# Optimization experiments

Hardware: AMD Instinct MI355X
Metric: run time of the kernel (lower is better)

Reference implementation:

```python
import jax, jax.numpy as jnp
import numpy as np

SUBSTEPS = 2  # fixed Tsit5 substeps per observation interval (replaces diffrax adaptive PID control)
# Tsit5 Butcher tableau (same stage math as diffrax.Tsit5)
C2, C3, C4, C5, C6 = 0.161, 0.327, 0.9, 0.9800255409045097, 1.0
A21 = 0.161
A31, A32 = -0.008480655492356989, 0.335480655492357
A41, A42, A43 = 2.8971530571054935, -6.359448489975075, 4.3622954328695815
A51, A52, A53, A54 = 5.325864828439257, -11.748883564062828, 7.4955393428898365, -0.09249506636175525
A61, A62, A63, A64, A65 = 5.86145544294642, -12.92096931784711, 8.159367898576159, -0.071584973281401, -0.028269050394068383
B1, B2, B3, B4, B5, B6 = 0.09646076681806523, 0.01, 0.4798896504144996, 1.379008574103742, -3.290069515436081, 2.324710524099774


def setup_inputs() -> dict:
    key = jax.random.key(0)
    ks = jax.random.split(key, 12)
    B, N, D_IN, H, ST, SW, OW, D_OUT = 128, 64, 32, 128, 16, 256, 256, 16

    def lin(k, o, i):
        return jax.random.normal(k, (o, i), jnp.float32) / np.sqrt(i).astype(np.float32)

    # strictly increasing timestamps with small intervals
    dts = jax.random.uniform(ks[0], (B, N), jnp.float32) * 0.05 + 0.01
    ts_batch = jnp.cumsum(dts, axis=1)
    X_batch = jax.random.normal(ks[1], (B, N, D_IN), jnp.float32)
    Static_batch = jax.random.normal(ks[2], (B, ST), jnp.float32)
    return dict(
        ts_batch=ts_batch, X_batch=X_batch, Static_batch=Static_batch,
        ode_w0=lin(ks[3], SW, 1 + H), ode_b0=jnp.zeros(SW, jnp.float32),
        ode_w1=lin(ks[4], SW, SW), ode_b1=jnp.zeros(SW, jnp.float32),
        ode_w2=lin(ks[5], H, SW), ode_b2=jnp.zeros(H, jnp.float32),
        ode_scale=jnp.array(1.0, jnp.float32),
        rnn_wh=lin(ks[6], H, H), rnn_wx=lin(ks[7], H, D_IN), rnn_bx=jnp.zeros(H, jnp.float32),
        inj_w=lin(ks[8], H, H + ST), inj_b=jnp.zeros(H, jnp.float32),
        out_w0=lin(ks[9], OW, H), out_b0=jnp.zeros(OW, jnp.float32),
        out_w1=lin(ks[10], OW, OW), out_b1=jnp.zeros(OW, jnp.float32),
        out_w2=lin(ks[11], D_OUT, OW), out_b2=jnp.zeros(D_OUT, jnp.float32),
    )


def reference(ts_batch, X_batch, Static_batch,
              ode_w0, ode_b0, ode_w1, ode_b1, ode_w2, ode_b2, ode_scale,
              rnn_wh, rnn_wx, rnn_bx, inj_w, inj_b,
              out_w0, out_b0, out_w1, out_b1, out_w2, out_b2):
    def f(t, h):  # vector field: t (B,), h (B,H)
        z = jnp.concatenate([t[:, None], h], axis=-1)
        z = jax.nn.silu(z @ ode_w0.T + ode_b0)
        z = jax.nn.silu(z @ ode_w1.T + ode_b1)
        return ode_scale * jnp.tanh(z @ ode_w2.T + ode_b2)

    def tsit5_step(t, dt, y):  # one Tsit5 step, batched over B
        d = dt[:, None]
        k1 = f(t, y)
        k2 = f(t + C2 * dt, y + d * (A21 * k1))
        k3 = f(t + C3 * dt, y + d * (A31 * k1 + A32 * k2))
        k4 = f(t + C4 * dt, y + d * (A41 * k1 + A42 * k2 + A43 * k3))
        k5 = f(t + C5 * dt, y + d * (A51 * k1 + A52 * k2 + A53 * k3 + A54 * k4))
        k6 = f(t + C6 * dt, y + d * (A61 * k1 + A62 * k2 + A63 * k3 + A64 * k4 + A65 * k5))
        return y + d * (B1 * k1 + B2 * k2 + B3 * k3 + B4 * k4 + B5 * k5 + B6 * k6)

    def ode_solve(t0, t1, y):  # fixed-substep Tsit5 integration from t0 to t1 (per-batch times)
        dt = (t1 - t0) / SUBSTEPS
        def body(yc, i):
            t = t0 + i.astype(t0.dtype) * dt
            return tsit5_step(t, dt, yc), None
        y, _ = jax.lax.scan(body, y, jnp.arange(SUBSTEPS))
        return y

    def rnn(h_prime, x):
        return jnp.tanh(h_prime @ rnn_wh.T + x @ rnn_wx.T + rnn_bx)

    # h0: rnn_cell(zeros, x0) -> inject static -> tanh
    h0 = jnp.tanh(X_batch[:, 0] @ rnn_wx.T + rnn_bx)  # hidden_linear(0) == 0
    h0 = jnp.tanh(jnp.concatenate([h0, Static_batch], axis=-1) @ inj_w.T + inj_b)

    xs = (ts_batch[:, :-1].T, ts_batch[:, 1:].T, jnp.swapaxes(X_batch[:, 1:], 0, 1))
    def step(h, inp):
        tp, tn, x = inp
        hp = ode_solve(tp, tn, h)
        return rnn(hp, x), None
    hN, _ = jax.lax.scan(step, h0, xs)

    z = jnp.tanh(hN @ out_w0.T + out_b0)
    z = jnp.tanh(z @ out_w1.T + out_b1)
    return z @ out_w2.T + out_b2  # (B, output_dim)
```

## Files before the change

### kernel.cpp

```cpp
#include <hip/hip_runtime.h>

typedef _Float16 f16;
typedef _Float16 f16x8 __attribute__((ext_vector_type(8)));
typedef float f32x4 __attribute__((ext_vector_type(4)));

#define MFMA16(a, b, c) __builtin_amdgcn_mfma_f32_16x16x32_f16((a), (b), (c), 0, 0, 0)

#define A21f 0.161f
#define A31f (-0.008480655492356989f)
#define A32f 0.335480655492357f
#define A41f 2.8971530571054935f
#define A42f (-6.359448489975075f)
#define A43f 4.3622954328695815f
#define A51f 5.325864828439257f
#define A52f (-11.748883564062828f)
#define A53f 7.4955393428898365f
#define A54f (-0.09249506636175525f)
#define A61f 5.86145544294642f
#define A62f (-12.92096931784711f)
#define A63f 8.159367898576159f
#define A64f (-0.071584973281401f)
#define A65f (-0.028269050394068383f)
#define B1f 0.09646076681806523f
#define B2f 0.01f
#define B3f 0.4798896504144996f
#define B4f 1.379008574103742f
#define B5f (-3.290069515436081f)
#define B6f 2.324710524099774f
#define C2f 0.161f
#define C3f 0.327f
#define C4f 0.9f
#define C5f 0.9800255409045097f
#define C6f 1.0f

#define PY 272
#define PZ 528
#define PX 80
#define PW 272
#define LDS_Y   0
#define LDS_Z1  4352
#define LDS_Z2  12800
#define LDS_X   21248
#define LDS_TS  22528
#define LDS_WH  26624
#define LDS_TOT 61440

__device__ __forceinline__ int yoff(int row, int bc)  { return LDS_Y  + row * PY + bc; }
__device__ __forceinline__ int z1off(int row, int bc) { return LDS_Z1 + row * PZ + bc; }
__device__ __forceinline__ int z2off(int row, int bc) { return LDS_Z2 + row * PZ + bc; }
__device__ __forceinline__ int xoff(int row, int bc)  { return LDS_X  + row * PX + bc; }
__device__ __forceinline__ int whoff(int row, int bc) { return LDS_WH + row * PW + bc; }

__device__ __forceinline__ float tanh_fast(float x) {
  return 2.0f * __builtin_amdgcn_rcpf(1.0f + __expf(-2.0f * x)) - 1.0f;
}
__device__ __forceinline__ float siluf(float x) {
  return x * __builtin_amdgcn_rcpf(1.0f + __expf(-x));
}

__global__ __launch_bounds__(512, 2)
void ode_rnn_kernel(const float* __restrict__ ts, const float* __restrict__ Xg,
                    const float* __restrict__ Sg,
                    const float* __restrict__ w0g, const float* __restrict__ b0g,
                    const float* __restrict__ w1g, const float* __restrict__ b1g,
                    const float* __restrict__ w2g, const float* __restrict__ b2g,
                    const float* __restrict__ scaleg,
                    const float* __restrict__ whg, const float* __restrict__ wxg,
                    const float* __restrict__ bxg,
                    const float* __restrict__ injwg, const float* __restrict__ injbg,
                    const float* __restrict__ ow0g, const float* __restrict__ ob0g,
                    const float* __restrict__ ow1g, const float* __restrict__ ob1g,
                    const float* __restrict__ ow2g, const float* __restrict__ ob2g,
                    float* __restrict__ outg) {
  const int t  = threadIdx.x;
  const int w  = t >> 6;
  const int l  = t & 63;
  const int lr = l & 15;
  const int lg = l >> 4;
  const int rb = blockIdx.x * 16;
  const int c1 = w * 32;
  const int c3 = w * 16;

  __shared__ __align__(16) unsigned char lds[LDS_TOT];

  for (int e = t; e < 16 * 64; e += 512) {
    *(float*)(lds + LDS_TS + e * 4) = ts[(size_t)(rb + (e >> 6)) * 64 + (e & 63)];
  }
  for (int e = t; e < 128 * 128; e += 512) {
    int r = e >> 7, c = e & 127;
    *(f16*)(lds + whoff(r, c * 2)) = (f16)whg[e];
  }
  {
    int r = t >> 5, d = t & 31;
    *(f16*)(lds + xoff(r, d * 2)) = (f16)Xg[(size_t)(rb + r) * 2048 + d];
  }
  if (t < 256) {
    int r = t >> 4, c = t & 15;
    *(f16*)(lds + z1off(r, (128 + c) * 2)) = (f16)Sg[(size_t)(rb + r) * 16 + c];
    *(f16*)(lds + z1off(r, (144 + c) * 2)) = (f16)0.0f;
  }

  float b0v[2], w0c0[2], b1v[2];
  #pragma unroll
  for (int nt = 0; nt < 2; ++nt) {
    int col = c1 + nt * 16 + lr;
    b0v[nt]  = b0g[col];
    w0c0[nt] = w0g[(size_t)col * 129];
    b1v[nt]  = b1g[col];
  }
  const float b2v = b2g[c3 + lr];
  const float bxv = bxg[c3 + lr];
  const float scalev = scaleg[0];

  auto ldfrag = [](const float* p) {
    f16x8 v;
    #pragma unroll
    for (int j = 0; j < 8; ++j) v[j] = (f16)p[j];
    return v;
  };

  f16x8 W0f[4][2];
  #pragma unroll
  for (int kt = 0; kt < 4; ++kt)
    #pragma unroll
    for (int nt = 0; nt < 2; ++nt)
      W0f[kt][nt] = ldfrag(w0g + (size_t)(c1 + nt * 16 + lr) * 129 + 1 + kt * 32 + lg * 8);

  f16x8 W1f[8][2];
  #pragma unroll
  for (int kt = 0; kt < 8; ++kt)
    #pragma unroll
    for (int nt = 0; nt < 2; ++nt)
      W1f[kt][nt] = ldfrag(w1g + (size_t)(c1 + nt * 16 + lr) * 256 + kt * 32 + lg * 8);

  f16x8 W2f[8];
  #pragma unroll
  for (int kt = 0; kt < 8; ++kt)
    W2f[kt] = ldfrag(w2g + (size_t)(c3 + lr) * 256 + kt * 32 + lg * 8);

  f16x8 WXf = ldfrag(wxg + (size_t)(c3 + lr) * 32 + lg * 8);

  __syncthreads();

  float y[4];
  float tpv[4], dv[4];

  auto writeY = [&](const float* yv) {
    #pragma unroll
    for (int r = 0; r < 4; ++r)
      *(f16*)(lds + yoff(lg * 4 + r, (c3 + lr) * 2)) = (f16)yv[r];
  };

  {
    f16x8 xa = *(const f16x8*)(lds + xoff(lr, lg * 16));
    f32x4 acc = {};
    acc = MFMA16(xa, WXf, acc);
    #pragma unroll
    for (int r = 0; r < 4; ++r) {
      float v = tanh_fast(acc[r] + bxv);
      *(f16*)(lds + z1off(lg * 4 + r, (c3 + lr) * 2)) = (f16)v;
    }
  }
  __syncthreads();
  {
    f16x8 af[5];
    #pragma unroll
    for (int kt = 0; kt < 5; ++kt) af[kt] = *(const f16x8*)(lds + z1off(lr, kt * 64 + lg * 16));
    f32x4 acc = {};
    int orow = c3 + lr;
    #pragma unroll
    for (int kt = 0; kt < 5; ++kt) {
      f16x8 bf;
      #pragma unroll
      for (int j = 0; j < 8; ++j) {
        int k = kt * 32 + lg * 8 + j;
        bf[j] = (k < 144) ? (f16)injwg[(size_t)orow * 144 + k] : (f16)0.0f;
      }
      acc = MFMA16(af[kt], bf, acc);
    }
    float ib = injbg[orow];
    #pragma unroll
    for (int r = 0; r < 4; ++r) y[r] = tanh_fast(acc[r] + ib);
  }
  writeY(y);
  __syncthreads();

  auto feval = [&](float sc, float* ko) {
    f16x8 af[8];
    #pragma unroll
    for (int kt = 0; kt < 4; ++kt) af[kt] = *(const f16x8*)(lds + yoff(lr, kt * 64 + lg * 16));
    f32x4 a1[2] = {}, a1b[2] = {};
    __builtin_amdgcn_s_setprio(1);
    #pragma unroll
    for (int kt = 0; kt < 2; ++kt)
      #pragma unroll
      for (int nt = 0; nt < 2; ++nt) {
        a1[nt]  = MFMA16(af[kt],     W0f[kt][nt],     a1[nt]);
        a1b[nt] = MFMA16(af[kt + 2], W0f[kt + 2][nt], a1b[nt]);
      }
    __builtin_amdgcn_s_setprio(0);
    #pragma unroll
    for (int nt = 0; nt < 2; ++nt)
      #pragma unroll
      for (int r = 0; r < 4; ++r) {
        float tr = tpv[r] + sc * dv[r];
        float v = siluf(a1[nt][r] + a1b[nt][r] + tr * w0c0[nt] + b0v[nt]);
        *(f16*)(lds + z1off(lg * 4 + r, (c1 + nt * 16 + lr) * 2)) = (f16)v;
      }
    __syncthreads();
    #pragma unroll
    for (int kt = 0; kt < 8; ++kt) af[kt] = *(const f16x8*)(lds + z1off(lr, kt * 64 + lg * 16));
    f32x4 a2[2] = {}, a2b[2] = {};
    __builtin_amdgcn_s_setprio(1);
    #pragma unroll
    for (int kt = 0; kt < 4; ++kt)
      #pragma unroll
      for (int nt = 0; nt < 2; ++nt) {
        a2[nt]  = MFMA16(af[kt],     W1f[kt][nt],     a2[nt]);
        a2b[nt] = MFMA16(af[kt + 4], W1f[kt + 4][nt], a2b[nt]);
      }
    __builtin_amdgcn_s_setprio(0);
    #pragma unroll
    for (int nt = 0; nt < 2; ++nt)
      #pragma unroll
      for (int r = 0; r < 4; ++r) {
        float v = siluf(a2[nt][r] + a2b[nt][r] + b1v[nt]);
        *(f16*)(lds + z2off(lg * 4 + r, (c1 + nt * 16 + lr) * 2)) = (f16)v;
      }
    __syncthreads();
    #pragma unroll
    for (int kt = 0; kt < 8; ++kt) af[kt] = *(const f16x8*)(lds + z2off(lr, kt * 64 + lg * 16));
    f32x4 a3 = {}, a3b = {}, a3c = {}, a3d = {};
    __builtin_amdgcn_s_setprio(1);
    #pragma unroll
    for (int kt = 0; kt < 2; ++kt) {
      a3  = MFMA16(af[kt],     W2f[kt],     a3);
      a3b = MFMA16(af[kt + 2], W2f[kt + 2], a3b);
      a3c = MFMA16(af[kt + 4], W2f[kt + 4], a3c);
      a3d = MFMA16(af[kt + 6], W2f[kt + 6], a3d);
    }
    __builtin_amdgcn_s_setprio(0);
    #pragma unroll
    for (int r = 0; r < 4; ++r)
      ko[r] = scalev * tanh_fast(((a3[r] + a3b[r]) + (a3c[r] + a3d[r])) + b2v);
  };

  #pragma unroll 1
  for (int n = 0; n < 63; ++n) {
    #pragma unroll
    for (int r = 0; r < 4; ++r) {
      float tp = *(const float*)(lds + LDS_TS + (((lg * 4 + r) * 64) + n) * 4);
      float tn = *(const float*)(lds + LDS_TS + (((lg * 4 + r) * 64) + n + 1) * 4);
      tpv[r] = tp;
      dv[r] = (tn - tp) * 0.5f;
    }
    {
      int r = t >> 5, d = t & 31;
      *(f16*)(lds + xoff(r, d * 2)) = (f16)Xg[(size_t)(rb + r) * 2048 + (size_t)(n + 1) * 32 + d];
    }

    #pragma unroll 1
    for (int s = 0; s < 2; ++s) {
      float k1v[4], k2v[4], k3v[4], k4v[4], k5v[4], k6v[4], yt[4];
      float sf = (float)s;
      feval(sf, k1v);
      #pragma unroll
      for (int i = 0; i < 4; ++i) yt[i] = y[i] + dv[i] * (A21f * k1v[i]);
      writeY(yt); __syncthreads();
      feval(sf + C2f, k2v);
      #pragma unroll
      for (int i = 0; i < 4; ++i) yt[i] = y[i] + dv[i] * (A31f * k1v[i] + A32f * k2v[i]);
      writeY(yt); __syncthreads();
      feval(sf + C3f, k3v);
      #pragma unroll
      for (int i = 0; i < 4; ++i) yt[i] = y[i] + dv[i] * (A41f * k1v[i] + A42f * k2v[i] + A43f * k3v[i]);
      writeY(yt); __syncthreads();
      feval(sf + C4f, k4v);
      #pragma unroll
      for (int i = 0; i < 4; ++i) yt[i] = y[i] + dv[i] * (A51f * k1v[i] + A52f * k2v[i] + A53f * k3v[i] + A54f * k4v[i]);
      writeY(yt); __syncthreads();
      feval(sf + C5f, k5v);
      #pragma unroll
      for (int i = 0; i < 4; ++i) yt[i] = y[i] + dv[i] * (A61f * k1v[i] + A62f * k2v[i] + A63f * k3v[i] + A64f * k4v[i] + A65f * k5v[i]);
      writeY(yt); __syncthreads();
      feval(sf + C6f, k6v);
      #pragma unroll
      for (int i = 0; i < 4; ++i)
        y[i] += dv[i] * (B1f * k1v[i] + B2f * k2v[i] + B3f * k3v[i] + B4f * k4v[i] + B5f * k5v[i] + B6f * k6v[i]);
      writeY(y); __syncthreads();
    }

    {
      f16x8 ha[4];
      #pragma unroll
      for (int kt = 0; kt < 4; ++kt) ha[kt] = *(const f16x8*)(lds + yoff(lr, kt * 64 + lg * 16));
      f16x8 xa = *(const f16x8*)(lds + xoff(lr, lg * 16));
      f32x4 acc = {}, accb = {};
      __builtin_amdgcn_s_setprio(1);
      #pragma unroll
      for (int kt = 0; kt < 2; ++kt) {
        f16x8 bf  = *(const f16x8*)(lds + whoff(c3 + lr, kt * 64 + lg * 16));
        f16x8 bf2 = *(const f16x8*)(lds + whoff(c3 + lr, (kt + 2) * 64 + lg * 16));
        acc  = MFMA16(ha[kt],     bf,  acc);
        accb = MFMA16(ha[kt + 2], bf2, accb);
      }
      acc = MFMA16(xa, WXf, acc);
      __builtin_amdgcn_s_setprio(0);
      #pragma unroll
      for (int r = 0; r < 4; ++r) y[r] = tanh_fast(acc[r] + accb[r] + bxv);
      writeY(y);
      __syncthreads();
    }
  }

  auto ldfrag2 = [](const float* p) {
    f16x8 v;
    #pragma unroll
    for (int j = 0; j < 8; ++j) v[j] = (f16)p[j];
    return v;
  };
  {
    f16x8 ha[4];
    #pragma unroll
    for (int kt = 0; kt < 4; ++kt) ha[kt] = *(const f16x8*)(lds + yoff(lr, kt * 64 + lg * 16));
    f32x4 acc[2] = {};
    #pragma unroll
    for (int kt = 0; kt < 4; ++kt)
      #pragma unroll
      for (int nt = 0; nt < 2; ++nt) {
        f16x8 bf = ldfrag2(ow0g + (size_t)(c1 + nt * 16 + lr) * 128 + kt * 32 + lg * 8);
        acc[nt] = MFMA16(ha[kt], bf, acc[nt]);
      }
    #pragma unroll
    for (int nt = 0; nt < 2; ++nt) {
      float bb = ob0g[c1 + nt * 16 + lr];
      #pragma unroll
      for (int r = 0; r < 4; ++r) {
        float v = tanh_fast(acc[nt][r] + bb);
        *(f16*)(lds + z1off(lg * 4 + r, (c1 + nt * 16 + lr) * 2)) = (f16)v;
      }
    }
  }
  __syncthreads();
  {
    f16x8 za[8];
    #pragma unroll
    for (int kt = 0; kt < 8; ++kt) za[kt] = *(const f16x8*)(lds + z1off(lr, kt * 64 + lg * 16));
    f32x4 acc[2] = {};
    #pragma unroll
    for (int kt = 0; kt < 8; ++kt)
      #pragma unroll
      for (int nt = 0; nt < 2; ++nt) {
        f16x8 bf = ldfrag2(ow1g + (size_t)(c1 + nt * 16 + lr) * 256 + kt * 32 + lg * 8);
        acc[nt] = MFMA16(za[kt], bf, acc[nt]);
      }
    #pragma unroll
    for (int nt = 0; nt < 2; ++nt) {
      float bb = ob1g[c1 + nt * 16 + lr];
      #pragma unroll
      for (int r = 0; r < 4; ++r) {
        float v = tanh_fast(acc[nt][r] + bb);
        *(f16*)(lds + z2off(lg * 4 + r, (c1 + nt * 16 + lr) * 2)) = (f16)v;
      }
    }
  }
  __syncthreads();
  if (w == 0) {
    f16x8 za[8];
    #pragma unroll
    for (int kt = 0; kt < 8; ++kt) za[kt] = *(const f16x8*)(lds + z2off(lr, kt * 64 + lg * 16));
    f32x4 acc = {};
    #pragma unroll
    for (int kt = 0; kt < 8; ++kt) {
      f16x8 bf = ldfrag2(ow2g + (size_t)lr * 256 + kt * 32 + lg * 8);
      acc = MFMA16(za[kt], bf, acc);
    }
    float bb = ob2g[lr];
    #pragma unroll
    for (int r = 0; r < 4; ++r)
      outg[(size_t)(rb + lg * 4 + r) * 16 + lr] = acc[r] + bb;
  }
}

extern "C" void kernel_launch(void* const* d_in, const int* in_sizes, int n_in,
                              void* d_out, int out_size, void* d_ws, size_t ws_size,
                              hipStream_t stream) {
  (void)in_sizes; (void)n_in; (void)d_ws; (void)ws_size; (void)out_size;
  ode_rnn_kernel<<<dim3(8), dim3(512), 0, stream>>>(
      (const float*)d_in[0],  (const float*)d_in[1],  (const float*)d_in[2],
      (const float*)d_in[3],  (const float*)d_in[4],  (const float*)d_in[5],
      (const float*)d_in[6],  (const float*)d_in[7],  (const float*)d_in[8],
      (const float*)d_in[9],  (const float*)d_in[10], (const float*)d_in[11],
      (const float*)d_in[12], (const float*)d_in[13], (const float*)d_in[14],
      (const float*)d_in[15], (const float*)d_in[16], (const float*)d_in[17],
      (const float*)d_in[18], (const float*)d_in[19], (const float*)d_in[20],
      (float*)d_out);
}
```

Before: 1.279 ms.

## Re-layout LDS activation and weight buffers into MFMA-fragment-contiguous blocks

Replaces the padded row-major LDS layouts for hidden state, intermediate activations, inputs and the recurrent weight with a blocked layout: 16 rows by 8 halves, stored so each lane's f16x8 fragment is one contiguous 16-byte chunk addressed by lane*16. Fragment reads become linear per wavefront and the scattered f16 writes are reorganised to match, aiming to cut LDS bank conflicts and address arithmetic in the latency-bound recurrent loop. The padding goes away, so LDS use shrinks a little. The scalar 2-byte stores remain and may still conflict.

```diff
diff --git a/kernel.cpp b/kernel.cpp
--- a/kernel.cpp
+++ b/kernel.cpp
@@ -33,23 +33,13 @@
 #define C5f 0.9800255409045097f
 #define C6f 1.0f
 
-#define PY 272
-#define PZ 528
-#define PX 80
-#define PW 272
 #define LDS_Y   0
-#define LDS_Z1  4352
-#define LDS_Z2  12800
-#define LDS_X   21248
-#define LDS_TS  22528
-#define LDS_WH  26624
-#define LDS_TOT 61440
-
-__device__ __forceinline__ int yoff(int row, int bc)  { return LDS_Y  + row * PY + bc; }
-__device__ __forceinline__ int z1off(int row, int bc) { return LDS_Z1 + row * PZ + bc; }
-__device__ __forceinline__ int z2off(int row, int bc) { return LDS_Z2 + row * PZ + bc; }
-__device__ __forceinline__ int xoff(int row, int bc)  { return LDS_X  + row * PX + bc; }
-__device__ __forceinline__ int whoff(int row, int bc) { return LDS_WH + row * PW + bc; }
+#define LDS_Z1  4096
+#define LDS_Z2  12288
+#define LDS_X   20480
+#define LDS_TS  21504
+#define LDS_WH  25600
+#define LDS_TOT 58368
 
 __device__ __forceinline__ float tanh_fast(float x) {
   return 2.0f * __builtin_amdgcn_rcpf(1.0f + __expf(-2.0f * x)) - 1.0f;
@@ -83,21 +73,28 @@
 
   __shared__ __align__(16) unsigned char lds[LDS_TOT];
 
+  const int ard  = l * 16;
+  const int whrd = LDS_WH + lg * 2048 + w * 256 + lr * 16;
+  const int zw   = w * 1024 + (lr >> 3) * 256 + lg * 64 + (lr & 7) * 2;
+  const int yw   = w * 512  + (lr >> 3) * 256 + lg * 64 + (lr & 7) * 2;
+
   for (int e = t; e < 16 * 64; e += 512) {
     *(float*)(lds + LDS_TS + e * 4) = ts[(size_t)(rb + (e >> 6)) * 64 + (e & 63)];
   }
   for (int e = t; e < 128 * 128; e += 512) {
-    int r = e >> 7, c = e & 127;
-    *(f16*)(lds + whoff(r, c * 2)) = (f16)whg[e];
+    int c = e >> 7, kk = e & 127;
+    *(f16*)(lds + LDS_WH + ((kk >> 3) * 128 + c) * 16 + (kk & 7) * 2) = (f16)whg[e];
   }
   {
     int r = t >> 5, d = t & 31;
-    *(f16*)(lds + xoff(r, d * 2)) = (f16)Xg[(size_t)(rb + r) * 2048 + d];
+    *(f16*)(lds + LDS_X + (d >> 3) * 256 + r * 16 + (d & 7) * 2) =
+        (f16)Xg[(size_t)(rb + r) * 2048 + d];
   }
   if (t < 256) {
     int r = t >> 4, c = t & 15;
-    *(f16*)(lds + z1off(r, (128 + c) * 2)) = (f16)Sg[(size_t)(rb + r) * 16 + c];
-    *(f16*)(lds + z1off(r, (144 + c) * 2)) = (f16)0.0f;
+    *(f16*)(lds + LDS_Z1 + 4096 + (c >> 3) * 256 + r * 16 + (c & 7) * 2) =
+        (f16)Sg[(size_t)(rb + r) * 16 + c];
+    *(f16*)(lds + LDS_Z1 + 4608 + (c >> 3) * 256 + r * 16 + (c & 7) * 2) = (f16)0.0f;
   }
 
   float b0v[2], w0c0[2], b1v[2];
@@ -148,24 +145,24 @@
   auto writeY = [&](const float* yv) {
     #pragma unroll
     for (int r = 0; r < 4; ++r)
-      *(f16*)(lds + yoff(lg * 4 + r, (c3 + lr) * 2)) = (f16)yv[r];
+      *(f16*)(lds + LDS_Y + yw + r * 16) = (f16)yv[r];
   };
 
   {
-    f16x8 xa = *(const f16x8*)(lds + xoff(lr, lg * 16));
+    f16x8 xa = *(const f16x8*)(lds + LDS_X + ard);
     f32x4 acc = {};
     acc = MFMA16(xa, WXf, acc);
     #pragma unroll
     for (int r = 0; r < 4; ++r) {
       float v = tanh_fast(acc[r] + bxv);
-      *(f16*)(lds + z1off(lg * 4 + r, (c3 + lr) * 2)) = (f16)v;
+      *(f16*)(lds + LDS_Z1 + yw + r * 16) = (f16)v;
     }
   }
   __syncthreads();
   {
     f16x8 af[5];
     #pragma unroll
-    for (int kt = 0; kt < 5; ++kt) af[kt] = *(const f16x8*)(lds + z1off(lr, kt * 64 + lg * 16));
+    for (int kt = 0; kt < 5; ++kt) af[kt] = *(const f16x8*)(lds + LDS_Z1 + ard + kt * 1024);
     f32x4 acc = {};
     int orow = c3 + lr;
     #pragma unroll
@@ -188,7 +185,7 @@
   auto feval = [&](float sc, float* ko) {
     f16x8 af[8];
     #pragma unroll
-    for (int kt = 0; kt < 4; ++kt) af[kt] = *(const f16x8*)(lds + yoff(lr, kt * 64 + lg * 16));
+    for (int kt = 0; kt < 4; ++kt) af[kt] = *(const f16x8*)(lds + LDS_Y + ard + kt * 1024);
     f32x4 a1[2] = {}, a1b[2] = {};
     __builtin_amdgcn_s_setprio(1);
     #pragma unroll
@@ -200,16 +197,17 @@
       }
     __builtin_amdgcn_s_setprio(0);
     #pragma unroll
-    for (int nt = 0; nt < 2; ++nt)
-      #pragma unroll
-      for (int r = 0; r < 4; ++r) {
-        float tr = tpv[r] + sc * dv[r];
+    for (int r = 0; r < 4; ++r) {
+      float tr = tpv[r] + sc * dv[r];
+      #pragma unroll
+      for (int nt = 0; nt < 2; ++nt) {
         float v = siluf(a1[nt][r] + a1b[nt][r] + tr * w0c0[nt] + b0v[nt]);
-        *(f16*)(lds + z1off(lg * 4 + r, (c1 + nt * 16 + lr) * 2)) = (f16)v;
-      }
+        *(f16*)(lds + LDS_Z1 + zw + nt * 512 + r * 16) = (f16)v;
+      }
+    }
     __syncthreads();
     #pragma unroll
-    for (int kt = 0; kt < 8; ++kt) af[kt] = *(const f16x8*)(lds + z1off(lr, kt * 64 + lg * 16));
+    for (int kt = 0; kt < 8; ++kt) af[kt] = *(const f16x8*)(lds + LDS_Z1 + ard + kt * 1024);
     f32x4 a2[2] = {}, a2b[2] = {};
     __builtin_amdgcn_s_setprio(1);
     #pragma unroll
@@ -225,11 +223,11 @@
       #pragma unroll
       for (int r = 0; r < 4; ++r) {
         float v = siluf(a2[nt][r] + a2b[nt][r] + b1v[nt]);
-        *(f16*)(lds + z2off(lg * 4 + r, (c1 + nt * 16 + lr) * 2)) = (f16)v;
+        *(f16*)(lds + LDS_Z2 + zw + nt * 512 + r * 16) = (f16)v;
       }
     __syncthreads();
     #pragma unroll
-    for (int kt = 0; kt < 8; ++kt) af[kt] = *(const f16x8*)(lds + z2off(lr, kt * 64 + lg * 16));
+    for (int kt = 0; kt < 8; ++kt) af[kt] = *(const f16x8*)(lds + LDS_Z2 + ard + kt * 1024);
     f32x4 a3 = {}, a3b = {}, a3c = {}, a3d = {};
     __builtin_amdgcn_s_setprio(1);
     #pragma unroll
@@ -256,7 +254,8 @@
     }
     {
       int r = t >> 5, d = t & 31;
-      *(f16*)(lds + xoff(r, d * 2)) = (f16)Xg[(size_t)(rb + r) * 2048 + (size_t)(n + 1) * 32 + d];
+      *(f16*)(lds + LDS_X + (d >> 3) * 256 + r * 16 + (d & 7) * 2) =
+          (f16)Xg[(size_t)(rb + r) * 2048 + (size_t)(n + 1) * 32 + d];
     }
 
     #pragma unroll 1
@@ -293,14 +292,14 @@
     {
       f16x8 ha[4];
       #pragma unroll
-      for (int kt = 0; kt < 4; ++kt) ha[kt] = *(const f16x8*)(lds + yoff(lr, kt * 64 + lg * 16));
-      f16x8 xa = *(const f16x8*)(lds + xoff(lr, lg * 16));
+      for (int kt = 0; kt < 4; ++kt) ha[kt] = *(const f16x8*)(lds + LDS_Y + ard + kt * 1024);
+      f16x8 xa = *(const f16x8*)(lds + LDS_X + ard);
       f32x4 acc = {}, accb = {};
       __builtin_amdgcn_s_setprio(1);
       #pragma unroll
       for (int kt = 0; kt < 2; ++kt) {
-        f16x8 bf  = *(const f16x8*)(lds + whoff(c3 + lr, kt * 64 + lg * 16));
-        f16x8 bf2 = *(const f16x8*)(lds + whoff(c3 + lr, (kt + 2) * 64 + lg * 16));
+        f16x8 bf  = *(const f16x8*)(lds + whrd + kt * 8192);
+        f16x8 bf2 = *(const f16x8*)(lds + whrd + (kt + 2) * 8192);
         acc  = MFMA16(ha[kt],     bf,  acc);
         accb = MFMA16(ha[kt + 2], bf2, accb);
       }
@@ -322,7 +321,7 @@
   {
     f16x8 ha[4];
     #pragma unroll
-    for (int kt = 0; kt < 4; ++kt) ha[kt] = *(const f16x8*)(lds + yoff(lr, kt * 64 + lg * 16));
+    for (int kt = 0; kt < 4; ++kt) ha[kt] = *(const f16x8*)(lds + LDS_Y + ard + kt * 1024);
     f32x4 acc[2] = {};
     #pragma unroll
     for (int kt = 0; kt < 4; ++kt)
@@ -337,7 +336,7 @@
       #pragma unroll
       for (int r = 0; r < 4; ++r) {
         float v = tanh_fast(acc[nt][r] + bb);
-        *(f16*)(lds + z1off(lg * 4 + r, (c1 + nt * 16 + lr) * 2)) = (f16)v;
+        *(f16*)(lds + LDS_Z1 + zw + nt * 512 + r * 16) = (f16)v;
       }
     }
   }
@@ -345,7 +344,7 @@
   {
     f16x8 za[8];
     #pragma unroll
-    for (int kt = 0; kt < 8; ++kt) za[kt] = *(const f16x8*)(lds + z1off(lr, kt * 64 + lg * 16));
+    for (int kt = 0; kt < 8; ++kt) za[kt] = *(const f16x8*)(lds + LDS_Z1 + ard + kt * 1024);
     f32x4 acc[2] = {};
     #pragma unroll
     for (int kt = 0; kt < 8; ++kt)
@@ -360,7 +359,7 @@
       #pragma unroll
       for (int r = 0; r < 4; ++r) {
         float v = tanh_fast(acc[nt][r] + bb);
-        *(f16*)(lds + z2off(lg * 4 + r, (c1 + nt * 16 + lr) * 2)) = (f16)v;
+        *(f16*)(lds + LDS_Z2 + zw + nt * 512 + r * 16) = (f16)v;
       }
     }
   }
@@ -368,7 +367,7 @@
   if (w == 0) {
     f16x8 za[8];
     #pragma unroll
-    for (int kt = 0; kt < 8; ++kt) za[kt] = *(const f16x8*)(lds + z2off(lr, kt * 64 + lg * 16));
+    for (int kt = 0; kt < 8; ++kt) za[kt] = *(const f16x8*)(lds + LDS_Z2 + ard + kt * 1024);
     f32x4 acc = {};
     #pragma unroll
     for (int kt = 0; kt < 8; ++kt) {
```

Result: faster. 1.225 ms (-4.2%).
